# Kernel optimization log

Hardware: AMD Instinct MI355X
Metric: run time of the kernel (lower is better)

## Reference

```python
import jax, jax.numpy as jnp
import numpy as np

EPS = 1e-11

def squash(s, axis=-1):
    sq = jnp.sum(s * s, axis=axis, keepdims=True)
    return (sq / (1.0 + sq)) * s / jnp.sqrt(sq + EPS)

def routing(u_hat, scale, num_iters=3):
    # u_hat: (b, P, J, D); dynamic routing (Sabour et al.), softmax over output capsules J
    b, P, J, D = u_hat.shape
    b_ij = jnp.zeros((b, P, J), u_hat.dtype)
    v = None
    for _ in range(num_iters):
        c = jax.nn.softmax(b_ij, axis=-1)
        s = jnp.einsum('bpj,bpjd->bjd', c, u_hat) / scale
        v = squash(s)
        b_ij = b_ij + jnp.einsum('bpjd,bjd->bpj', u_hat, v)
    return v

def normalize_adj(adj):
    deg = jnp.sum(adj, axis=-1)
    d_inv_sqrt = jnp.where(deg > 0, deg ** -0.5, 0.0)
    return d_inv_sqrt[:, :, None] * adj * d_inv_sqrt[:, None, :]

def setup_inputs():
    key = jax.random.key(0)
    ks = jax.random.split(key, 20)
    b, n = 32, 512
    vocabs = [128, 64, 16]
    emb, C, L = 64, 2, 3
    hidden = emb * C                 # 128
    gcn_in = emb * len(vocabs)       # 192
    att_dim = emb * C * L            # 384
    Jg, Dg = 16, 32                  # num_graph_capsules, graph_embedding_size
    ncls = 6
    recon_hidden = int(gcn_in * 2 / 3)  # 128
    recon_dim = 208
    g = lambda i, *s: jax.random.normal(ks[i], s, jnp.float32) * 0.05
    # sparse symmetric adjacency with self-loops (binary, like real graph data)
    adj = (jax.random.uniform(ks[0], (b, n, n)) < 0.02).astype(jnp.float32)
    adj = jnp.maximum(adj, jnp.swapaxes(adj, 1, 2))
    adj = jnp.maximum(adj, jnp.eye(n, dtype=jnp.float32)[None])
    return {
        'adj': adj,
        'nodes0': jax.random.randint(ks[1], (b, n), 0, vocabs[0]),
        'nodes1': jax.random.randint(ks[2], (b, n), 0, vocabs[1]),
        'nodes2': jax.random.randint(ks[3], (b, n), 0, vocabs[2]),
        'label': jax.random.randint(ks[4], (b,), 0, ncls),
        'reconstructs': jax.random.uniform(ks[5], (b, recon_dim)),
        'emb0': g(6, vocabs[0], emb), 'emb1': g(7, vocabs[1], emb), 'emb2': g(8, vocabs[2], emb),
        'gw0': g(9, gcn_in, hidden), 'gb0': jnp.zeros((hidden,), jnp.float32),
        'gw1': g(10, hidden, hidden), 'gb1': jnp.zeros((hidden,), jnp.float32),
        'gw2': g(11, hidden, hidden), 'gb2': jnp.zeros((hidden,), jnp.float32),
        'aw1': g(12, att_dim, att_dim), 'ab1': jnp.zeros((att_dim,), jnp.float32),
        'aw2': g(13, att_dim, 1), 'ab2': jnp.zeros((1,), jnp.float32),
        'Wg': g(14, C * L, emb, Jg, Dg),
        'Wc': g(15, Jg, Dg, ncls, Dg),
        'rw1': g(16, Dg, recon_hidden), 'rb1': jnp.zeros((recon_hidden,), jnp.float32),
        'rw2': g(17, recon_hidden, recon_dim), 'rb2': jnp.zeros((recon_dim,), jnp.float32),
    }

def reference(adj, nodes0, nodes1, nodes2, label, reconstructs,
              emb0, emb1, emb2, gw0, gb0, gw1, gb1, gw2, gb2,
              aw1, ab1, aw2, ab2, Wg, Wc, rw1, rb1, rw2, rb2):
    b, n, _ = adj.shape
    C = 2
    lambda_val, reg_scale = 0.5, 0.1
    # embeddings (dropout omitted: eval-mode reference)
    feats = jnp.concatenate([emb0[nodes0], emb1[nodes1], emb2[nodes2]], axis=-1)  # (b,n,192)
    masks = jnp.max(adj, axis=-1, keepdims=True)                    # (b,n,1)
    num_nodes = jnp.sum(masks, axis=1, keepdims=True)[..., None]    # (b,1,1,1)
    adj_norm = normalize_adj(adj)
    hid = []
    h = feats
    for W, bb in ((gw0, gb0), (gw1, gb1), (gw2, gb2)):
        h = jnp.tanh(jnp.einsum('bnm,bmd->bnd', adj_norm, h @ W + bb))
        hid.append(h.reshape(b, n, C, -1))
    H = jnp.concatenate(hid, axis=2)                                # (b,n,C*L,emb)
    attn = jnp.tanh(H.reshape(b, n, -1) @ aw1 + ab1) @ aw2 + ab2    # (b,n,1)
    attn = jax.nn.softmax(jnp.where(masks > 0, attn, -jnp.inf), axis=1)[..., None]
    H = H * attn * num_nodes
    # graph capsules: every (node, channel) is an input capsule
    Jg, Dg = Wg.shape[2], Wg.shape[3]
    u_hat = jnp.einsum('bnci,cijd->bncjd', H, Wg).reshape(b, n * Wg.shape[0], Jg, Dg)
    v_g = routing(u_hat, num_nodes.reshape(b, 1, 1))                # (b,Jg,Dg)
    u_hat2 = jnp.einsum('bci,cijd->bcjd', v_g, Wc)
    v_c = routing(u_hat2, 1.0)                                      # (b,ncls,Dg)
    # margin loss
    v_mag = jnp.sqrt(jnp.sum(v_c * v_c, axis=2))
    pred = jnp.argmax(v_mag, axis=1)
    max_l = jnp.maximum(0.9 - v_mag, 0.0) ** 2
    max_r = jnp.maximum(v_mag - 0.1, 0.0) ** 2
    T_c = jax.nn.one_hot(label, v_mag.shape[1], dtype=v_c.dtype)
    L_c = jnp.sum(T_c * max_l + lambda_val * (1.0 - T_c) * max_r, axis=1)
    margin_loss = jnp.mean(L_c)
    # reconstruction loss
    capsule_masked = jnp.sum(v_c * T_c[..., None], axis=1)          # (b,Dg)
    rec = jax.nn.sigmoid(jax.nn.relu(capsule_masked @ rw1 + rb1) @ rw2 + rb2)
    neg_ind = (reconstructs < 1e-05).astype(rec.dtype)
    pos_ind = 1.0 - neg_ind
    rec_val = reconstructs / (jnp.max(reconstructs, axis=1, keepdims=True) + EPS)
    diff = (rec - rec_val) ** 2
    recon_loss = jnp.mean(jnp.max(diff * pos_ind, axis=-1) + jnp.max(diff * neg_ind, axis=-1))
    loss = margin_loss + recon_loss * reg_scale
    return (v_c, loss, margin_loss, recon_loss, pred)
```

## Files before the change

### kernel.cpp

```cpp
#include <hip/hip_runtime.h>
#include <hip/hip_bf16.h>
#include <math.h>

#define NB 32
#define NN 512
#define GIN 192
#define ATT 384
#define EPSF 1e-11f

typedef __attribute__((ext_vector_type(4))) float f32x4;
typedef __attribute__((ext_vector_type(8))) short short8;

__device__ __forceinline__ ushort bfhi(float f) {
    uint u = __float_as_uint(f);
    return (ushort)((u + 0x7FFFu + ((u >> 16) & 1u)) >> 16);
}
__device__ __forceinline__ float bff(ushort h) {
    return __uint_as_float(((uint)h) << 16);
}
__device__ __forceinline__ void bfsplit(float f, ushort& hi, ushort& lo) {
    hi = bfhi(f);
    lo = bfhi(f - bff(hi));
}

__global__ __launch_bounds__(64) void k_prep(const float* __restrict__ adj,
                                             ushort* __restrict__ nbr,
                                             int* __restrict__ deg,
                                             float* __restrict__ dinv,
                                             float* __restrict__ mask) {
    int row = blockIdx.x;
    int t = threadIdx.x;
    const float* a = adj + (size_t)row * NN;
    float4 v0 = ((const float4*)a)[t * 2];
    float4 v1 = ((const float4*)a)[t * 2 + 1];
    float vv[8] = {v0.x, v0.y, v0.z, v0.w, v1.x, v1.y, v1.z, v1.w};
    float s = 0.f, m = 0.f;
    int cnt = 0;
    unsigned long long below = (t == 63) ? 0xFFFFFFFFFFFFFFFFULL >> 1
                                         : ((1ULL << t) - 1ULL);
#pragma unroll
    for (int e = 0; e < 8; e++) {
        float v = vv[e];
        s += v;
        m = fmaxf(m, v);
        bool nz = v != 0.f;
        unsigned long long bm = __ballot(nz);
        int pos = cnt + __popcll(bm & below);
        if (nz && pos < 64) nbr[(size_t)row * 64 + pos] = (ushort)(t * 8 + e);
        cnt += __popcll(bm);
    }
    for (int off = 32; off; off >>= 1) {
        s += __shfl_xor(s, off);
        m = fmaxf(m, __shfl_xor(m, off));
    }
    if (t == 0) {
        deg[row] = cnt < 64 ? cnt : 64;
        dinv[row] = s > 0.f ? 1.0f / sqrtf(s) : 0.f;
        mask[row] = m;
    }
}

__global__ void k_gather(const int* __restrict__ n0, const int* __restrict__ n1,
                         const int* __restrict__ n2, const float* __restrict__ e0,
                         const float* __restrict__ e1, const float* __restrict__ e2,
                         ushort* __restrict__ fh, ushort* __restrict__ fl) {
    int tid = blockIdx.x * 256 + threadIdx.x;
    if (tid >= NB * NN * GIN) return;
    int bn = tid / GIN, f = tid - bn * GIN;
    float v;
    if (f < 64)       v = e0[n0[bn] * 64 + f];
    else if (f < 128) v = e1[n1[bn] * 64 + (f - 64)];
    else              v = e2[n2[bn] * 64 + (f - 128)];
    ushort h, lo;
    bfsplit(v, h, lo);
    fh[tid] = h; fl[tid] = lo;
}

__global__ __launch_bounds__(256) void k_twtall(
    const float* __restrict__ gw0, const float* __restrict__ gw1,
    const float* __restrict__ gw2, const float* __restrict__ aw1,
    ushort* __restrict__ t0h, ushort* __restrict__ t0l,
    ushort* __restrict__ t1h, ushort* __restrict__ t1l,
    ushort* __restrict__ t2h, ushort* __restrict__ t2l,
    ushort* __restrict__ tah, ushort* __restrict__ tal) {
    const float* W; ushort *Th, *Tl; int K, N;
    switch (blockIdx.z) {
        case 0: W = gw0; Th = t0h; Tl = t0l; K = 192; N = 128; break;
        case 1: W = gw1; Th = t1h; Tl = t1l; K = 128; N = 128; break;
        case 2: W = gw2; Th = t2h; Tl = t2l; K = 128; N = 128; break;
        default: W = aw1; Th = tah; Tl = tal; K = 384; N = 384; break;
    }
    int k0 = blockIdx.x * 32, n0 = blockIdx.y * 32;
    if (k0 >= K || n0 >= N) return;
    __shared__ float tile[32][33];
    int t = threadIdx.x, tx = t & 31, ty = t >> 5;
#pragma unroll
    for (int r = 0; r < 4; r++)
        tile[ty + r * 8][tx] = W[(size_t)(k0 + ty + r * 8) * N + n0 + tx];
    __syncthreads();
#pragma unroll
    for (int r = 0; r < 4; r++) {
        int nn = ty + r * 8;
        float v = tile[tx][nn];
        ushort h, lo;
        bfsplit(v, h, lo);
        size_t o = (size_t)(n0 + nn) * K + k0 + tx;
        Th[o] = h; Tl[o] = lo;
    }
}

template <int KK, int EPI>
__global__ __launch_bounds__(256) void k_mfg(
    const ushort* __restrict__ Ah, const ushort* __restrict__ Al, int lda,
    const ushort* __restrict__ Bh, const ushort* __restrict__ Bl,
    const float* __restrict__ bias, const float* __restrict__ dinv,
    float* __restrict__ Of, const float* __restrict__ aw2p) {
    __shared__ ushort Ash[2048], Asl[2048];
    __shared__ ushort Bsh[4096], Bsl[4096];
    __shared__ float ep[(EPI == 0) ? 64 * 128 : 1];
    int t = threadIdx.x;
    int bid = blockIdx.x;
    {
        int q = gridDim.x >> 3;
        bid = (bid & 7) * q + (bid >> 3);
    }
    int m0 = bid * 64;
    int n0 = blockIdx.y * 128;
    int l = t & 63, w = t >> 6, wr = w >> 1, wc = w & 1;
    int rA = t >> 2, kc = t & 3;
    int rB0 = rA, rB1 = rA + 64;
    int lsA  = ((rA >> 4) * 64 + (rA & 15) + kc * 16) * 8;
    int lsB0 = ((rB0 >> 4) * 64 + (rB0 & 15) + kc * 16) * 8;
    int lsB1 = ((rB1 >> 4) * 64 + (rB1 & 15) + kc * 16) * 8;
    f32x4 z = {0.f, 0.f, 0.f, 0.f};
    f32x4 acc[2][4];
#pragma unroll
    for (int i = 0; i < 2; i++)
#pragma unroll
        for (int j = 0; j < 4; j++) acc[i][j] = z;

    short8 pa0, pal0, pb0, pb1, pbl0, pbl1;
    int kof = kc * 8;
    {
        pa0 = *(const short8*)&Ah[(size_t)(m0 + rA) * lda + kof];
        pal0 = *(const short8*)&Al[(size_t)(m0 + rA) * lda + kof];
        pb0 = *(const short8*)&Bh[(size_t)(n0 + rB0) * KK + kof];
        pb1 = *(const short8*)&Bh[(size_t)(n0 + rB1) * KK + kof];
        pbl0 = *(const short8*)&Bl[(size_t)(n0 + rB0) * KK + kof];
        pbl1 = *(const short8*)&Bl[(size_t)(n0 + rB1) * KK + kof];
    }
    for (int k0 = 0; k0 < KK; k0 += 32) {
        *(short8*)&Ash[lsA] = pa0;
        *(short8*)&Asl[lsA] = pal0;
        *(short8*)&Bsh[lsB0] = pb0;
        *(short8*)&Bsh[lsB1] = pb1;
        *(short8*)&Bsl[lsB0] = pbl0;
        *(short8*)&Bsl[lsB1] = pbl1;
        __syncthreads();
        if (k0 + 32 < KK) {
            int kn = k0 + 32 + kof;
            pa0 = *(const short8*)&Ah[(size_t)(m0 + rA) * lda + kn];
            pal0 = *(const short8*)&Al[(size_t)(m0 + rA) * lda + kn];
            pb0 = *(const short8*)&Bh[(size_t)(n0 + rB0) * KK + kn];
            pb1 = *(const short8*)&Bh[(size_t)(n0 + rB1) * KK + kn];
            pbl0 = *(const short8*)&Bl[(size_t)(n0 + rB0) * KK + kn];
            pbl1 = *(const short8*)&Bl[(size_t)(n0 + rB1) * KK + kn];
        }
        short8 ah[2], al[2], bh[4], bl[4];
#pragma unroll
        for (int i = 0; i < 2; i++) {
            ah[i] = *(const short8*)&Ash[((wr * 2 + i) * 64 + l) * 8];
            al[i] = *(const short8*)&Asl[((wr * 2 + i) * 64 + l) * 8];
        }
#pragma unroll
        for (int j = 0; j < 4; j++) {
            bh[j] = *(const short8*)&Bsh[((wc * 4 + j) * 64 + l) * 8];
            bl[j] = *(const short8*)&Bsl[((wc * 4 + j) * 64 + l) * 8];
        }
#pragma unroll
        for (int i = 0; i < 2; i++)
#pragma unroll
            for (int j = 0; j < 4; j++) {
                acc[i][j] = __builtin_amdgcn_mfma_f32_16x16x32_bf16(ah[i], bh[j], acc[i][j], 0, 0, 0);
                acc[i][j] = __builtin_amdgcn_mfma_f32_16x16x32_bf16(ah[i], bl[j], acc[i][j], 0, 0, 0);
                acc[i][j] = __builtin_amdgcn_mfma_f32_16x16x32_bf16(al[i], bh[j], acc[i][j], 0, 0, 0);
            }
        __syncthreads();
    }
    if constexpr (EPI == 3) {
#pragma unroll
        for (int i = 0; i < 2; i++) {
            float rs[4] = {0.f, 0.f, 0.f, 0.f};
#pragma unroll
            for (int j = 0; j < 4; j++) {
                int gc = n0 + (wc * 4 + j) * 16 + (l & 15);
                float bv = bias[gc], wv = aw2p[gc];
#pragma unroll
                for (int r = 0; r < 4; r++)
                    rs[r] += tanhf(acc[i][j][r] + bv) * wv;
            }
#pragma unroll
            for (int r = 0; r < 4; r++) {
                rs[r] += __shfl_xor(rs[r], 1, 16);
                rs[r] += __shfl_xor(rs[r], 2, 16);
                rs[r] += __shfl_xor(rs[r], 4, 16);
                rs[r] += __shfl_xor(rs[r], 8, 16);
            }
            if ((l & 15) == 0) {
                int gr0 = m0 + (wr * 2 + i) * 16 + 4 * (l >> 4);
#pragma unroll
                for (int r = 0; r < 4; r++) atomicAdd(&Of[gr0 + r], rs[r]);
            }
        }
    } else {
#pragma unroll
        for (int i = 0; i < 2; i++)
#pragma unroll
            for (int j = 0; j < 4; j++) {
                int lc = (wc * 4 + j) * 16 + (l & 15);
                int lr0 = (wr * 2 + i) * 16 + 4 * (l >> 4);
                float bv = bias[lc];
#pragma unroll
                for (int r = 0; r < 4; r++)
                    ep[(lr0 + r) * 128 + lc] = (acc[i][j][r] + bv) * dinv[m0 + lr0 + r];
            }
        __syncthreads();
        int row = t >> 2, c0 = (t & 3) * 32;
        size_t ob = (size_t)(m0 + row) * 128 + c0;
#pragma unroll
        for (int k = 0; k < 8; k++)
            ((float4*)&Of[ob])[k] = *(const float4*)&ep[row * 128 + c0 + k * 4];
    }
}

__global__ __launch_bounds__(256) void k_adjsp(const ushort* __restrict__ nbr,
                                               const int* __restrict__ deg,
                                               const float* __restrict__ Y,
                                               const float* __restrict__ dinv,
                                               ushort* __restrict__ Hbh,
                                               ushort* __restrict__ Hbl, int hoff) {
    int bid = blockIdx.x;
    {
        int q = gridDim.x >> 3;
        bid = (bid & 7) * q + (bid >> 3);
    }
    int b = bid >> 5;
    int rg = bid & 31;
    int base = b * NN + rg * 16;
    __shared__ ushort nl[16 * 64];
    __shared__ int dl[16];
    int t = threadIdx.x;
    if (t < 128) *(short8*)&nl[t * 8] = *(const short8*)&nbr[(size_t)base * 64 + t * 8];
    if (t < 16) dl[t] = deg[base + t];
    __syncthreads();
    int row = t >> 4, c0 = (t & 15) * 8;
    const float* yp = Y + (size_t)b * 65536 + c0;
    float acc[8] = {0.f, 0.f, 0.f, 0.f, 0.f, 0.f, 0.f, 0.f};
    int dg = dl[row];
    const ushort* nr = &nl[row * 64];
    for (int q = 0; q < dg; q++) {
        const float4* y = (const float4*)(yp + (int)nr[q] * 128);
        float4 a = y[0], c = y[1];
        acc[0] += a.x; acc[1] += a.y; acc[2] += a.z; acc[3] += a.w;
        acc[4] += c.x; acc[5] += c.y; acc[6] += c.z; acc[7] += c.w;
    }
    float dv = dinv[base + row];
    short8 vh, vl;
#pragma unroll
    for (int c = 0; c < 8; c++) {
        float v = tanhf(acc[c] * dv);
        ushort h, lo;
        bfsplit(v, h, lo);
        vh[c] = (short)h; vl[c] = (short)lo;
    }
    size_t o = (size_t)(base + row) * ATT + hoff + c0;
    *(short8*)&Hbh[o] = vh;
    *(short8*)&Hbl[o] = vl;
}

__global__ __launch_bounds__(512) void k_attnsm(float* __restrict__ logit,
                                                const float* __restrict__ mask,
                                                float* __restrict__ numn) {
    __shared__ float red[8], red2[8], red3[8];
    int b = blockIdx.x, t = threadIdx.x;
    float mk = mask[b * NN + t];
    float x = mk > 0.f ? logit[b * NN + t] : -INFINITY;
    float m = x, nsum = mk;
    for (int off = 32; off; off >>= 1) {
        m = fmaxf(m, __shfl_xor(m, off));
        nsum += __shfl_xor(nsum, off);
    }
    if ((t & 63) == 0) { red[t >> 6] = m; red3[t >> 6] = nsum; }
    __syncthreads();
    float gm = red[0], nn = red3[0];
    for (int i = 1; i < 8; i++) { gm = fmaxf(gm, red[i]); nn += red3[i]; }
    float e = expf(x - gm);
    float s = e;
    for (int off = 32; off; off >>= 1) s += __shfl_xor(s, off);
    if ((t & 63) == 0) red2[t >> 6] = s;
    __syncthreads();
    float gs = 0.f;
    for (int i = 0; i < 8; i++) gs += red2[i];
    logit[b * NN + t] = (e / gs) * nn;
    if (t == 0) numn[b] = nn;
}

__global__ __launch_bounds__(256) void k_Hsum(const ushort* __restrict__ Hh,
                                              const ushort* __restrict__ Hl,
                                              const float* __restrict__ scale,
                                              float* __restrict__ G0) {
    int blk = blockIdx.x;
    int c = blk % 6, b = blk / 6;
    int t = threadIdx.x;
    int i = t & 63, g = t >> 6;
    float s = 0.f;
    for (int n = g * 128; n < g * 128 + 128; n++) {
        size_t o = ((size_t)b * NN + n) * ATT + c * 64 + i;
        s += scale[b * NN + n] * (bff(Hh[o]) + bff(Hl[o]));
    }
    __shared__ float red[256];
    red[t] = s;
    __syncthreads();
    if (t < 128) red[t] += red[t + 128];
    __syncthreads();
    if (t < 64) G0[(size_t)blk * 64 + i] = red[t] + red[t + 64];
}

template <int SRC, bool DOWV>
__global__ __launch_bounds__(256) void k_SVj(const float* __restrict__ gsrc,
                                             const float* __restrict__ Wg,
                                             const float* __restrict__ numn,
                                             float* __restrict__ vg,
                                             float* __restrict__ Wv) {
    int b = blockIdx.x, j = blockIdx.y;
    int t = threadIdx.x;
    __shared__ float Wgl[384 * 33];
    __shared__ float gj[384];
    __shared__ float red[256];
    __shared__ float vvs[32];
    for (int idx = t; idx < 12288; idx += 256) {
        int r = idx >> 5, d = idx & 31;
        Wgl[r * 33 + d] = Wg[(size_t)r * 512 + j * 32 + d];
    }
    for (int r = t; r < 384; r += 256) {
        if constexpr (SRC == 0) {
            gj[r] = gsrc[b * 384 + r] * (1.f / 16.f);
        } else {
            const float* g = gsrc + ((size_t)b * 6 + (r >> 6)) * 4096 + j * 64 + (r & 63);
            gj[r] = g[0] + g[1024] + g[2048] + g[3072];
        }
    }
    __syncthreads();
    int d = t & 31, g8 = t >> 5;
    float pp = 0.f;
#pragma unroll
    for (int k = 0; k < 48; k++) {
        int r = g8 * 48 + k;
        pp += gj[r] * Wgl[r * 33 + d];
    }
    red[t] = pp;
    __syncthreads();
    if (t < 128) red[t] += red[t + 128];
    __syncthreads();
    if (t < 64) red[t] += red[t + 64];
    __syncthreads();
    if (t < 32) {
        float s = (red[t] + red[t + 32]) / numn[b];
        float sq = s * s;
        for (int off = 16; off; off >>= 1) sq += __shfl_xor(sq, off, 32);
        float v = (sq / (1.f + sq)) * s / sqrtf(sq + EPSF);
        vvs[t] = v;
        vg[(size_t)b * 512 + j * 32 + t] = v;
    }
    __syncthreads();
    if constexpr (DOWV) {
        for (int r = t; r < 384; r += 256) {
            float a = 0.f;
#pragma unroll
            for (int d2 = 0; d2 < 32; d2++) a += Wgl[r * 33 + d2] * vvs[d2];
            Wv[(size_t)b * 6144 + (r >> 6) * 1024 + (r & 63) * 16 + j] = a;
        }
    }
}

__global__ __launch_bounds__(256) void k_GsSM(const float* __restrict__ bij,
                                              const ushort* __restrict__ Hh,
                                              const ushort* __restrict__ Hl,
                                              const float* __restrict__ scale,
                                              float* __restrict__ Gs) {
    int blk = blockIdx.x;
    int seg = blk & 3, c = (blk >> 2) % 6, b = blk / 24;
    __shared__ float ct[16 * 16];
    __shared__ float ht[16 * 64];
    int t = threadIdx.x;
    int i = t & 63, j0 = t >> 6;
    float acc[4] = {0.f, 0.f, 0.f, 0.f};
    int n0 = seg * 128;
    for (int nc = 0; nc < 128; nc += 16) {
        {
            int nn = t >> 4;
            float v = bij[(((size_t)b * NN + n0 + nc + nn) * 6 + c) * 16 + (t & 15)];
            float mx = v;
            mx = fmaxf(mx, __shfl_xor(mx, 1, 16));
            mx = fmaxf(mx, __shfl_xor(mx, 2, 16));
            mx = fmaxf(mx, __shfl_xor(mx, 4, 16));
            mx = fmaxf(mx, __shfl_xor(mx, 8, 16));
            float e = expf(v - mx);
            float sm = e;
            sm += __shfl_xor(sm, 1, 16);
            sm += __shfl_xor(sm, 2, 16);
            sm += __shfl_xor(sm, 4, 16);
            sm += __shfl_xor(sm, 8, 16);
            ct[t] = e / sm;
        }
        for (int idx = t; idx < 1024; idx += 256) {
            int nn = idx >> 6, ii = idx & 63;
            int n = n0 + nc + nn;
            size_t o = ((size_t)b * NN + n) * ATT + c * 64 + ii;
            ht[idx] = scale[b * NN + n] * (bff(Hh[o]) + bff(Hl[o]));
        }
        __syncthreads();
        for (int nn = 0; nn < 16; nn++) {
            float hv = ht[nn * 64 + i];
#pragma unroll
            for (int q = 0; q < 4; q++) acc[q] += ct[nn * 16 + j0 * 4 + q] * hv;
        }
        __syncthreads();
    }
#pragma unroll
    for (int q = 0; q < 4; q++) {
        int j = j0 * 4 + q;
        Gs[(((size_t)b * 6 + c) * 4 + seg) * 1024 + j * 64 + i] = acc[q];
    }
}

template <bool ACC>
__global__ __launch_bounds__(256) void k_bup(const ushort* __restrict__ Hh,
                                             const ushort* __restrict__ Hl,
                                             const float* __restrict__ scale,
                                             const float* __restrict__ Wv,
                                             float* __restrict__ bij) {
    int blk = blockIdx.x;
    int b = blk >> 4;
    int n0 = (blk & 15) * 32;
    __shared__ float wl[6144];
    __shared__ float hl[32 * ATT];
    int t = threadIdx.x;
    for (int idx = t; idx < 6144; idx += 256) wl[idx] = Wv[(size_t)b * 6144 + idx];
    for (int idx = t; idx < 32 * ATT; idx += 256) {
        int nn = idx / ATT;
        size_t o = ((size_t)b * NN + n0) * ATT + idx;
        hl[idx] = scale[b * NN + n0 + nn] * (bff(Hh[o]) + bff(Hl[o]));
    }
    __syncthreads();
    for (int idx = t; idx < 3072; idx += 256) {
        int nn = idx / 96, r = idx % 96, c = r >> 4, j = r & 15;
        float a = 0.f;
        const float* h = hl + nn * ATT + c * 64;
        const float* w = wl + c * 1024 + j;
#pragma unroll
        for (int i2 = 0; i2 < 64; i2++) a += h[i2] * w[i2 * 16];
        size_t o = (((size_t)b * NN + n0 + nn) * 6 + c) * 16 + j;
        if constexpr (ACC) bij[o] += a;
        else bij[o] = a;
    }
}

__global__ __launch_bounds__(256) void k_u2(const float* __restrict__ vg,
                                            const float* __restrict__ Wc,
                                            float* __restrict__ u2g) {
    int c = blockIdx.x;
    int t = threadIdx.x;
    __shared__ float Wcl[32 * 192];
    __shared__ float vgl[32 * 32];
    for (int idx = t; idx < 6144; idx += 256)
        Wcl[idx] = Wc[(size_t)c * 6144 + idx];
    for (int idx = t; idx < 1024; idx += 256) {
        int b = idx >> 5, i2 = idx & 31;
        vgl[idx] = vg[(size_t)b * 512 + c * 32 + i2];
    }
    __syncthreads();
    for (int o = t; o < 6144; o += 256) {
        int b = o / 192, jd = o - b * 192;
        float a = 0.f;
#pragma unroll
        for (int i2 = 0; i2 < 32; i2++) a += vgl[b * 32 + i2] * Wcl[i2 * 192 + jd];
        u2g[(size_t)b * 3072 + c * 192 + jd] = a;
    }
}

__global__ __launch_bounds__(256) void k_caps2(
    const float* __restrict__ u2g,
    const int* __restrict__ label, const float* __restrict__ recon_in,
    const float* __restrict__ rw1, const float* __restrict__ rb1,
    const float* __restrict__ rw2, const float* __restrict__ rb2,
    float* __restrict__ out, float* __restrict__ marg, float* __restrict__ reconl) {
    int b = blockIdx.x, t = threadIdx.x;
    __shared__ float u2[3072];
    __shared__ float b2[96], c2b[96];
    __shared__ float vv[192];
    __shared__ float magl[6];
    __shared__ float cm[32];
    __shared__ float hidl[128];
    __shared__ float red[256];
    for (int idx = t; idx < 3072; idx += 256) u2[idx] = u2g[(size_t)b * 3072 + idx];
    if (t < 96) b2[t] = 0.f;
    __syncthreads();
    for (int it = 0; it < 3; it++) {
        if (t < 16) {
            float mx = -INFINITY;
            for (int j = 0; j < 6; j++) mx = fmaxf(mx, b2[t * 6 + j]);
            float e[6], s = 0.f;
            for (int j = 0; j < 6; j++) { e[j] = expf(b2[t * 6 + j] - mx); s += e[j]; }
            for (int j = 0; j < 6; j++) c2b[t * 6 + j] = e[j] / s;
        }
        __syncthreads();
        if (t < 192) {
            int j = t >> 5, d = t & 31;
            float s = 0.f;
            for (int c = 0; c < 16; c++) s += c2b[c * 6 + j] * u2[c * 192 + j * 32 + d];
            float sq = s * s;
            for (int off = 16; off; off >>= 1) sq += __shfl_xor(sq, off, 32);
            vv[t] = (sq / (1.f + sq)) * s / sqrtf(sq + EPSF);
        }
        __syncthreads();
        if (it < 2) {
            if (t < 96) {
                int c = t / 6, j = t - c * 6;
                float a = 0.f;
                for (int d = 0; d < 32; d++) a += u2[c * 192 + j * 32 + d] * vv[j * 32 + d];
                b2[t] += a;
            }
            __syncthreads();
        }
    }
    if (t < 192) out[(size_t)b * 192 + t] = vv[t];
    if (t < 6) {
        float s = 0.f;
        for (int d = 0; d < 32; d++) { float v = vv[t * 32 + d]; s += v * v; }
        magl[t] = sqrtf(s);
    }
    __syncthreads();
    int lab = label[b];
    if (t == 0) {
        float L = 0.f;
        int p = 0;
        float best = magl[0];
        for (int j = 0; j < 6; j++) {
            float mg = magl[j];
            if (mg > best) { best = mg; p = j; }
            float ml = fmaxf(0.9f - mg, 0.f); ml *= ml;
            float mr = fmaxf(mg - 0.1f, 0.f); mr *= mr;
            L += (j == lab) ? ml : 0.5f * mr;
        }
        marg[b] = L;
        out[6147 + b] = (float)p;
    }
    if (t < 32) cm[t] = vv[lab * 32 + t];
    __syncthreads();
    if (t < 128) {
        float a = rb1[t];
        for (int d = 0; d < 32; d++) a += cm[d] * rw1[d * 128 + t];
        hidl[t] = fmaxf(a, 0.f);
    }
    __syncthreads();
    bool act = t < 208;
    float rv = 0.f, rin = 0.f;
    if (act) {
        float a = rb2[t];
        for (int k = 0; k < 128; k++) a += hidl[k] * rw2[k * 208 + t];
        rv = 1.f / (1.f + expf(-a));
        rin = recon_in[(size_t)b * 208 + t];
    }
    red[t] = act ? rin : -INFINITY;
    __syncthreads();
    for (int s2 = 128; s2; s2 >>= 1) {
        if (t < s2) red[t] = fmaxf(red[t], red[t + s2]);
        __syncthreads();
    }
    float rmax = red[0];
    __syncthreads();
    float dpos = 0.f, dneg = 0.f;
    if (act) {
        float rec_val = rin / (rmax + EPSF);
        float d2 = rv - rec_val; d2 *= d2;
        bool neg = rin < 1e-5f;
        dpos = neg ? 0.f : d2;
        dneg = neg ? d2 : 0.f;
    }
    red[t] = dpos;
    __syncthreads();
    for (int s2 = 128; s2; s2 >>= 1) {
        if (t < s2) red[t] = fmaxf(red[t], red[t + s2]);
        __syncthreads();
    }
    float mp = red[0];
    __syncthreads();
    red[t] = dneg;
    __syncthreads();
    for (int s2 = 128; s2; s2 >>= 1) {
        if (t < s2) red[t] = fmaxf(red[t], red[t + s2]);
        __syncthreads();
    }
    if (t == 0) reconl[b] = mp + red[0];
}

__global__ void k_final(const float* __restrict__ marg, const float* __restrict__ reconl,
                        float* __restrict__ out) {
    int t = threadIdx.x;
    float m = (t < 32) ? marg[t] : 0.f;
    float r = (t < 32) ? reconl[t] : 0.f;
    for (int off = 16; off; off >>= 1) { m += __shfl_xor(m, off, 32); r += __shfl_xor(r, off, 32); }
    if (t == 0) {
        m /= 32.f;
        r /= 32.f;
        out[6144] = m + 0.1f * r;
        out[6145] = m;
        out[6146] = r;
    }
}

extern "C" void kernel_launch(void* const* d_in, const int* in_sizes, int n_in,
                              void* d_out, int out_size, void* d_ws, size_t ws_size,
                              hipStream_t stream) {
    const float* adj   = (const float*)d_in[0];
    const int*   n0    = (const int*)d_in[1];
    const int*   n1    = (const int*)d_in[2];
    const int*   n2    = (const int*)d_in[3];
    const int*   label = (const int*)d_in[4];
    const float* recon = (const float*)d_in[5];
    const float* e0    = (const float*)d_in[6];
    const float* e1    = (const float*)d_in[7];
    const float* e2    = (const float*)d_in[8];
    const float* gw0   = (const float*)d_in[9];
    const float* gb0   = (const float*)d_in[10];
    const float* gw1   = (const float*)d_in[11];
    const float* gb1   = (const float*)d_in[12];
    const float* gw2   = (const float*)d_in[13];
    const float* gb2   = (const float*)d_in[14];
    const float* aw1   = (const float*)d_in[15];
    const float* ab1   = (const float*)d_in[16];
    const float* aw2   = (const float*)d_in[17];
    const float* Wg    = (const float*)d_in[19];
    const float* Wc    = (const float*)d_in[20];
    const float* rw1   = (const float*)d_in[21];
    const float* rb1   = (const float*)d_in[22];
    const float* rw2   = (const float*)d_in[23];
    const float* rb2   = (const float*)d_in[24];
    float* out = (float*)d_out;

    char* p = (char*)d_ws;
    auto alloc = [&](size_t bytes) { char* r = p; p += (bytes + 255) & ~(size_t)255; return r; };
    float*  dinv   = (float*)alloc(NB * NN * 4);
    float*  maskp  = (float*)alloc(NB * NN * 4);
    float*  numn   = (float*)alloc(NB * 4);
    float*  logit  = (float*)alloc(NB * NN * 4);
    float*  bij    = (float*)alloc((size_t)NB * NN * 96 * 4);
    float*  Gs     = (float*)alloc((size_t)NB * 24576 * 4);
    float*  G0     = (float*)alloc(NB * 384 * 4);
    float*  vg     = (float*)alloc(NB * 512 * 4);
    float*  Wv     = (float*)alloc(NB * 6144 * 4);
    float*  u2g    = (float*)alloc(NB * 3072 * 4);
    float*  marg   = (float*)alloc(NB * 4);
    float*  recl   = (float*)alloc(NB * 4);
    int*    deg    = (int*)alloc(NB * NN * 4);
    ushort* nbr    = (ushort*)alloc((size_t)NB * NN * 64 * 2);
    ushort* gwt0h  = (ushort*)alloc(128 * 192 * 2);
    ushort* gwt0l  = (ushort*)alloc(128 * 192 * 2);
    ushort* gwt1h  = (ushort*)alloc(128 * 128 * 2);
    ushort* gwt1l  = (ushort*)alloc(128 * 128 * 2);
    ushort* gwt2h  = (ushort*)alloc(128 * 128 * 2);
    ushort* gwt2l  = (ushort*)alloc(128 * 128 * 2);
    ushort* aw1th  = (ushort*)alloc(384 * 384 * 2);
    ushort* aw1tl  = (ushort*)alloc(384 * 384 * 2);
    float*  Ybuf   = (float*)alloc((size_t)NB * NN * 128 * 4);
    ushort* Hbh    = (ushort*)alloc((size_t)NB * NN * ATT * 2);
    ushort* Hbl    = (ushort*)alloc((size_t)NB * NN * ATT * 2);
    ushort* fbh    = (ushort*)alloc((size_t)NB * NN * GIN * 2);
    ushort* fbl    = (ushort*)alloc((size_t)NB * NN * GIN * 2);

    k_prep<<<NB * NN, 64, 0, stream>>>(adj, nbr, deg, dinv, maskp);
    k_gather<<<(NB * NN * GIN + 255) / 256, 256, 0, stream>>>(n0, n1, n2, e0, e1, e2, fbh, fbl);
    k_twtall<<<dim3(12, 12, 4), 256, 0, stream>>>(gw0, gw1, gw2, aw1, gwt0h, gwt0l,
                                                  gwt1h, gwt1l, gwt2h, gwt2l, aw1th, aw1tl);

    k_mfg<192, 0><<<256, 256, 0, stream>>>(fbh, fbl, 192, gwt0h, gwt0l, gb0, dinv, Ybuf, nullptr);
    k_adjsp<<<1024, 256, 0, stream>>>(nbr, deg, Ybuf, dinv, Hbh, Hbl, 0);
    k_mfg<128, 0><<<256, 256, 0, stream>>>(Hbh, Hbl, ATT, gwt1h, gwt1l, gb1, dinv, Ybuf, nullptr);
    k_adjsp<<<1024, 256, 0, stream>>>(nbr, deg, Ybuf, dinv, Hbh, Hbl, 128);
    k_mfg<128, 0><<<256, 256, 0, stream>>>(Hbh + 128, Hbl + 128, ATT, gwt2h, gwt2l, gb2, dinv, Ybuf, nullptr);
    k_adjsp<<<1024, 256, 0, stream>>>(nbr, deg, Ybuf, dinv, Hbh, Hbl, 256);

    hipMemsetAsync(logit, 0, NB * NN * sizeof(float), stream);
    k_mfg<384, 3><<<dim3(256, 3), 256, 0, stream>>>(Hbh, Hbl, ATT, aw1th, aw1tl, ab1, nullptr,
                                                    logit, aw2);
    k_attnsm<<<NB, 512, 0, stream>>>(logit, maskp, numn);

    k_Hsum<<<NB * 6, 256, 0, stream>>>(Hbh, Hbl, logit, G0);
    k_SVj<0, true><<<dim3(NB, 16), 256, 0, stream>>>(G0, Wg, numn, vg, Wv);
    k_bup<false><<<NB * 16, 256, 0, stream>>>(Hbh, Hbl, logit, Wv, bij);
    k_GsSM<<<NB * 24, 256, 0, stream>>>(bij, Hbh, Hbl, logit, Gs);
    k_SVj<1, true><<<dim3(NB, 16), 256, 0, stream>>>(Gs, Wg, numn, vg, Wv);
    k_bup<true><<<NB * 16, 256, 0, stream>>>(Hbh, Hbl, logit, Wv, bij);
    k_GsSM<<<NB * 24, 256, 0, stream>>>(bij, Hbh, Hbl, logit, Gs);
    k_SVj<1, false><<<dim3(NB, 16), 256, 0, stream>>>(Gs, Wg, numn, vg, nullptr);

    k_u2<<<16, 256, 0, stream>>>(vg, Wc, u2g);
    k_caps2<<<NB, 256, 0, stream>>>(u2g, label, recon, rw1, rb1, rw2, rb2, out, marg, recl);
    k_final<<<1, 64, 0, stream>>>(marg, recl, out);
}
```

Baseline: 414.3 us.

## Fuse front-end prep kernels and merge routing tail into one cooperative kernel

```diff
diff --git a/kernel.cpp b/kernel.cpp
--- a/kernel.cpp
+++ b/kernel.cpp
@@ -1,6 +1,9 @@
 #include <hip/hip_runtime.h>
 #include <hip/hip_bf16.h>
+#include <hip/hip_cooperative_groups.h>
 #include <math.h>
+
+namespace cg = cooperative_groups;
 
 #define NB 32
 #define NN 512
@@ -23,89 +26,87 @@
     lo = bfhi(f - bff(hi));
 }
 
-__global__ __launch_bounds__(64) void k_prep(const float* __restrict__ adj,
-                                             ushort* __restrict__ nbr,
-                                             int* __restrict__ deg,
-                                             float* __restrict__ dinv,
-                                             float* __restrict__ mask) {
-    int row = blockIdx.x;
-    int t = threadIdx.x;
-    const float* a = adj + (size_t)row * NN;
-    float4 v0 = ((const float4*)a)[t * 2];
-    float4 v1 = ((const float4*)a)[t * 2 + 1];
-    float vv[8] = {v0.x, v0.y, v0.z, v0.w, v1.x, v1.y, v1.z, v1.w};
-    float s = 0.f, m = 0.f;
-    int cnt = 0;
-    unsigned long long below = (t == 63) ? 0xFFFFFFFFFFFFFFFFULL >> 1
-                                         : ((1ULL << t) - 1ULL);
-#pragma unroll
-    for (int e = 0; e < 8; e++) {
-        float v = vv[e];
-        s += v;
-        m = fmaxf(m, v);
-        bool nz = v != 0.f;
-        unsigned long long bm = __ballot(nz);
-        int pos = cnt + __popcll(bm & below);
-        if (nz && pos < 64) nbr[(size_t)row * 64 + pos] = (ushort)(t * 8 + e);
-        cnt += __popcll(bm);
-    }
-    for (int off = 32; off; off >>= 1) {
-        s += __shfl_xor(s, off);
-        m = fmaxf(m, __shfl_xor(m, off));
-    }
-    if (t == 0) {
-        deg[row] = cnt < 64 ? cnt : 64;
-        dinv[row] = s > 0.f ? 1.0f / sqrtf(s) : 0.f;
-        mask[row] = m;
-    }
-}
-
-__global__ void k_gather(const int* __restrict__ n0, const int* __restrict__ n1,
-                         const int* __restrict__ n2, const float* __restrict__ e0,
-                         const float* __restrict__ e1, const float* __restrict__ e2,
-                         ushort* __restrict__ fh, ushort* __restrict__ fl) {
-    int tid = blockIdx.x * 256 + threadIdx.x;
-    if (tid >= NB * NN * GIN) return;
-    int bn = tid / GIN, f = tid - bn * GIN;
-    float v;
-    if (f < 64)       v = e0[n0[bn] * 64 + f];
-    else if (f < 128) v = e1[n1[bn] * 64 + (f - 64)];
-    else              v = e2[n2[bn] * 64 + (f - 128)];
-    ushort h, lo;
-    bfsplit(v, h, lo);
-    fh[tid] = h; fl[tid] = lo;
-}
-
-__global__ __launch_bounds__(256) void k_twtall(
+__global__ __launch_bounds__(256) void k_front(
+    const float* __restrict__ adj, ushort* __restrict__ nbr, int* __restrict__ deg,
+    float* __restrict__ dinv, float* __restrict__ mask,
+    const int* __restrict__ n0, const int* __restrict__ n1, const int* __restrict__ n2,
+    const float* __restrict__ e0, const float* __restrict__ e1, const float* __restrict__ e2,
+    ushort* __restrict__ fh, ushort* __restrict__ fl,
     const float* __restrict__ gw0, const float* __restrict__ gw1,
     const float* __restrict__ gw2, const float* __restrict__ aw1,
     ushort* __restrict__ t0h, ushort* __restrict__ t0l,
     ushort* __restrict__ t1h, ushort* __restrict__ t1l,
     ushort* __restrict__ t2h, ushort* __restrict__ t2l,
     ushort* __restrict__ tah, ushort* __restrict__ tal) {
-    const float* W; ushort *Th, *Tl; int K, N;
-    switch (blockIdx.z) {
-        case 0: W = gw0; Th = t0h; Tl = t0l; K = 192; N = 128; break;
-        case 1: W = gw1; Th = t1h; Tl = t1l; K = 128; N = 128; break;
-        case 2: W = gw2; Th = t2h; Tl = t2l; K = 128; N = 128; break;
-        default: W = aw1; Th = tah; Tl = tal; K = 384; N = 384; break;
-    }
-    int k0 = blockIdx.x * 32, n0 = blockIdx.y * 32;
-    if (k0 >= K || n0 >= N) return;
     __shared__ float tile[32][33];
-    int t = threadIdx.x, tx = t & 31, ty = t >> 5;
-#pragma unroll
-    for (int r = 0; r < 4; r++)
-        tile[ty + r * 8][tx] = W[(size_t)(k0 + ty + r * 8) * N + n0 + tx];
-    __syncthreads();
-#pragma unroll
-    for (int r = 0; r < 4; r++) {
-        int nn = ty + r * 8;
-        float v = tile[tx][nn];
+    int blk = blockIdx.x, t = threadIdx.x;
+    if (blk < 4096) {
+        int row = blk * 4 + (t >> 6);
+        int lane = t & 63;
+        const float* a = adj + (size_t)row * NN;
+        float4 v0 = ((const float4*)a)[lane * 2];
+        float4 v1 = ((const float4*)a)[lane * 2 + 1];
+        float vv[8] = {v0.x, v0.y, v0.z, v0.w, v1.x, v1.y, v1.z, v1.w};
+        float s = 0.f, m = 0.f;
+        int cnt = 0;
+        unsigned long long below = (lane == 63) ? 0xFFFFFFFFFFFFFFFFULL >> 1
+                                                : ((1ULL << lane) - 1ULL);
+#pragma unroll
+        for (int e = 0; e < 8; e++) {
+            float v = vv[e];
+            s += v;
+            m = fmaxf(m, v);
+            bool nz = v != 0.f;
+            unsigned long long bm = __ballot(nz);
+            int pos = cnt + __popcll(bm & below);
+            if (nz && pos < 64) nbr[(size_t)row * 64 + pos] = (ushort)(lane * 8 + e);
+            cnt += __popcll(bm);
+        }
+        for (int off = 32; off; off >>= 1) {
+            s += __shfl_xor(s, off);
+            m = fmaxf(m, __shfl_xor(m, off));
+        }
+        if (lane == 0) {
+            deg[row] = cnt < 64 ? cnt : 64;
+            dinv[row] = s > 0.f ? 1.0f / sqrtf(s) : 0.f;
+            mask[row] = m;
+        }
+    } else if (blk < 16384) {
+        int tid = (blk - 4096) * 256 + t;
+        int bn = tid / GIN, f = tid - bn * GIN;
+        float v;
+        if (f < 64)       v = e0[n0[bn] * 64 + f];
+        else if (f < 128) v = e1[n1[bn] * 64 + (f - 64)];
+        else              v = e2[n2[bn] * 64 + (f - 128)];
         ushort h, lo;
         bfsplit(v, h, lo);
-        size_t o = (size_t)(n0 + nn) * K + k0 + tx;
-        Th[o] = h; Tl[o] = lo;
+        fh[tid] = h; fl[tid] = lo;
+    } else {
+        int job = blk - 16384;
+        int z = job / 144, rem = job % 144;
+        int k0 = (rem / 12) * 32, nn0 = (rem % 12) * 32;
+        const float* W; ushort *Th, *Tl; int K, N;
+        switch (z) {
+            case 0: W = gw0; Th = t0h; Tl = t0l; K = 192; N = 128; break;
+            case 1: W = gw1; Th = t1h; Tl = t1l; K = 128; N = 128; break;
+            case 2: W = gw2; Th = t2h; Tl = t2l; K = 128; N = 128; break;
+            default: W = aw1; Th = tah; Tl = tal; K = 384; N = 384; break;
+        }
+        if (k0 >= K || nn0 >= N) return;
+        int tx = t & 31, ty = t >> 5;
+#pragma unroll
+        for (int r = 0; r < 4; r++)
+            tile[ty + r * 8][tx] = W[(size_t)(k0 + ty + r * 8) * N + nn0 + tx];
+        __syncthreads();
+#pragma unroll
+        for (int r = 0; r < 4; r++) {
+            int nn = ty + r * 8;
+            float v = tile[tx][nn];
+            ushort h, lo;
+            bfsplit(v, h, lo);
+            size_t o = (size_t)(nn0 + nn) * K + k0 + tx;
+            Th[o] = h; Tl[o] = lo;
+        }
     }
 }
 
@@ -278,76 +279,75 @@
     *(short8*)&Hbl[o] = vl;
 }
 
-__global__ __launch_bounds__(512) void k_attnsm(float* __restrict__ logit,
-                                                const float* __restrict__ mask,
-                                                float* __restrict__ numn) {
-    __shared__ float red[8], red2[8], red3[8];
-    int b = blockIdx.x, t = threadIdx.x;
-    float mk = mask[b * NN + t];
-    float x = mk > 0.f ? logit[b * NN + t] : -INFINITY;
-    float m = x, nsum = mk;
+struct RArgs {
+    float* logit; const float* maskp; float* numn;
+    const ushort* Hbh; const ushort* Hbl;
+    float* G0; const float* Wg; float* vg; float* Wv;
+    float* bij; float* Gs; float* u2g; const float* Wc;
+    const int* label; const float* recon;
+    const float* rw1; const float* rb1; const float* rw2; const float* rb2;
+    float* out; float* marg; float* recl;
+};
+
+__device__ void ph_attnsm(const RArgs& a, int b, int t, float* pool) {
+    float* red = pool; float* red2 = pool + 4; float* red3 = pool + 8;
+    float mk0 = a.maskp[b * NN + t], mk1 = a.maskp[b * NN + 256 + t];
+    float x0 = mk0 > 0.f ? a.logit[b * NN + t] : -INFINITY;
+    float x1 = mk1 > 0.f ? a.logit[b * NN + 256 + t] : -INFINITY;
+    float m = fmaxf(x0, x1), ns = mk0 + mk1;
     for (int off = 32; off; off >>= 1) {
         m = fmaxf(m, __shfl_xor(m, off));
-        nsum += __shfl_xor(nsum, off);
-    }
-    if ((t & 63) == 0) { red[t >> 6] = m; red3[t >> 6] = nsum; }
-    __syncthreads();
-    float gm = red[0], nn = red3[0];
-    for (int i = 1; i < 8; i++) { gm = fmaxf(gm, red[i]); nn += red3[i]; }
-    float e = expf(x - gm);
-    float s = e;
+        ns += __shfl_xor(ns, off);
+    }
+    if ((t & 63) == 0) { red[t >> 6] = m; red3[t >> 6] = ns; }
+    __syncthreads();
+    float gm = fmaxf(fmaxf(red[0], red[1]), fmaxf(red[2], red[3]));
+    float nn = red3[0] + red3[1] + red3[2] + red3[3];
+    float e0 = expf(x0 - gm), e1 = expf(x1 - gm);
+    float s = e0 + e1;
     for (int off = 32; off; off >>= 1) s += __shfl_xor(s, off);
     if ((t & 63) == 0) red2[t >> 6] = s;
     __syncthreads();
-    float gs = 0.f;
-    for (int i = 0; i < 8; i++) gs += red2[i];
-    logit[b * NN + t] = (e / gs) * nn;
-    if (t == 0) numn[b] = nn;
-}
-
-__global__ __launch_bounds__(256) void k_Hsum(const ushort* __restrict__ Hh,
-                                              const ushort* __restrict__ Hl,
-                                              const float* __restrict__ scale,
-                                              float* __restrict__ G0) {
-    int blk = blockIdx.x;
-    int c = blk % 6, b = blk / 6;
-    int t = threadIdx.x;
-    int i = t & 63, g = t >> 6;
+    float gs = red2[0] + red2[1] + red2[2] + red2[3];
+    a.logit[b * NN + t] = (e0 / gs) * nn;
+    a.logit[b * NN + 256 + t] = (e1 / gs) * nn;
+    if (t == 0) a.numn[b] = nn;
+    __syncthreads();
+}
+
+__device__ void ph_Hsum(const RArgs& a, int job, int t, float* pool) {
+    int c = job % 6, b = job / 6;
+    int i = t & 63, gq = t >> 6;
     float s = 0.f;
-    for (int n = g * 128; n < g * 128 + 128; n++) {
+    for (int n = gq * 128; n < gq * 128 + 128; n++) {
         size_t o = ((size_t)b * NN + n) * ATT + c * 64 + i;
-        s += scale[b * NN + n] * (bff(Hh[o]) + bff(Hl[o]));
-    }
-    __shared__ float red[256];
+        s += a.logit[b * NN + n] * (bff(a.Hbh[o]) + bff(a.Hbl[o]));
+    }
+    float* red = pool;
     red[t] = s;
     __syncthreads();
     if (t < 128) red[t] += red[t + 128];
     __syncthreads();
-    if (t < 64) G0[(size_t)blk * 64 + i] = red[t] + red[t + 64];
+    if (t < 64) a.G0[(size_t)job * 64 + i] = red[t] + red[t + 64];
+    __syncthreads();
 }
 
 template <int SRC, bool DOWV>
-__global__ __launch_bounds__(256) void k_SVj(const float* __restrict__ gsrc,
-                                             const float* __restrict__ Wg,
-                                             const float* __restrict__ numn,
-                                             float* __restrict__ vg,
-                                             float* __restrict__ Wv) {
-    int b = blockIdx.x, j = blockIdx.y;
-    int t = threadIdx.x;
-    __shared__ float Wgl[384 * 33];
-    __shared__ float gj[384];
-    __shared__ float red[256];
-    __shared__ float vvs[32];
+__device__ void ph_SVj(const RArgs& a, int b, int j, int t, float* pool) {
+    float* Wgl = pool;
+    float* gj  = pool + 12672;
+    float* red = pool + 13056;
+    float* vvs = pool + 13312;
     for (int idx = t; idx < 12288; idx += 256) {
         int r = idx >> 5, d = idx & 31;
-        Wgl[r * 33 + d] = Wg[(size_t)r * 512 + j * 32 + d];
+        Wgl[r * 33 + d] = a.Wg[(size_t)r * 512 + j * 32 + d];
     }
     for (int r = t; r < 384; r += 256) {
         if constexpr (SRC == 0) {
-            gj[r] = gsrc[b * 384 + r] * (1.f / 16.f);
+            gj[r] = a.G0[b * 384 + r] * (1.f / 16.f);
         } else {
-            const float* g = gsrc + ((size_t)b * 6 + (r >> 6)) * 4096 + j * 64 + (r & 63);
-            gj[r] = g[0] + g[1024] + g[2048] + g[3072];
+            const float* gp = a.Gs + ((size_t)b * 6 + (r >> 6)) * 4096 + j * 64 + (r & 63);
+            gj[r] = gp[0] + gp[1024] + gp[2048] + gp[3072];
         }
     }
     __syncthreads();
@@ -365,41 +365,63 @@
     if (t < 64) red[t] += red[t + 64];
     __syncthreads();
     if (t < 32) {
-        float s = (red[t] + red[t + 32]) / numn[b];
+        float s = (red[t] + red[t + 32]) / a.numn[b];
         float sq = s * s;
         for (int off = 16; off; off >>= 1) sq += __shfl_xor(sq, off, 32);
         float v = (sq / (1.f + sq)) * s / sqrtf(sq + EPSF);
         vvs[t] = v;
-        vg[(size_t)b * 512 + j * 32 + t] = v;
+        a.vg[(size_t)b * 512 + j * 32 + t] = v;
     }
     __syncthreads();
     if constexpr (DOWV) {
         for (int r = t; r < 384; r += 256) {
-            float a = 0.f;
-#pragma unroll
-            for (int d2 = 0; d2 < 32; d2++) a += Wgl[r * 33 + d2] * vvs[d2];
-            Wv[(size_t)b * 6144 + (r >> 6) * 1024 + (r & 63) * 16 + j] = a;
-        }
-    }
-}
-
-__global__ __launch_bounds__(256) void k_GsSM(const float* __restrict__ bij,
-                                              const ushort* __restrict__ Hh,
-                                              const ushort* __restrict__ Hl,
-                                              const float* __restrict__ scale,
-                                              float* __restrict__ Gs) {
-    int blk = blockIdx.x;
-    int seg = blk & 3, c = (blk >> 2) % 6, b = blk / 24;
-    __shared__ float ct[16 * 16];
-    __shared__ float ht[16 * 64];
-    int t = threadIdx.x;
+            float s2 = 0.f;
+#pragma unroll
+            for (int d2 = 0; d2 < 32; d2++) s2 += Wgl[r * 33 + d2] * vvs[d2];
+            a.Wv[(size_t)b * 6144 + (r >> 6) * 1024 + (r & 63) * 16 + j] = s2;
+        }
+    }
+    __syncthreads();
+}
+
+template <bool ACC>
+__device__ void ph_bup16(const RArgs& a, int job, int t, float* pool) {
+    int b = job >> 5;
+    int n0 = (job & 31) * 16;
+    float* wl = pool;
+    float* hl = pool + 6144;
+    for (int idx = t; idx < 6144; idx += 256) wl[idx] = a.Wv[(size_t)b * 6144 + idx];
+    for (int idx = t; idx < 6144; idx += 256) {
+        int nn = idx / ATT;
+        size_t o = ((size_t)b * NN + n0) * ATT + idx;
+        hl[idx] = a.logit[b * NN + n0 + nn] * (bff(a.Hbh[o]) + bff(a.Hbl[o]));
+    }
+    __syncthreads();
+    for (int idx = t; idx < 1536; idx += 256) {
+        int nn = idx / 96, r = idx % 96, c = r >> 4, j = r & 15;
+        float s = 0.f;
+        const float* h = hl + nn * ATT + c * 64;
+        const float* w = wl + c * 1024 + j;
+#pragma unroll
+        for (int i2 = 0; i2 < 64; i2++) s += h[i2] * w[i2 * 16];
+        size_t o = (((size_t)b * NN + n0 + nn) * 6 + c) * 16 + j;
+        if constexpr (ACC) a.bij[o] += s;
+        else a.bij[o] = s;
+    }
+    __syncthreads();
+}
+
+__device__ void ph_GsSM(const RArgs& a, int job, int t, float* pool) {
+    int seg = job & 3, c = (job >> 2) % 6, b = job / 24;
+    float* ct = pool;
+    float* ht = pool + 256;
     int i = t & 63, j0 = t >> 6;
     float acc[4] = {0.f, 0.f, 0.f, 0.f};
     int n0 = seg * 128;
     for (int nc = 0; nc < 128; nc += 16) {
         {
             int nn = t >> 4;
-            float v = bij[(((size_t)b * NN + n0 + nc + nn) * 6 + c) * 16 + (t & 15)];
+            float v = a.bij[(((size_t)b * NN + n0 + nc + nn) * 6 + c) * 16 + (t & 15)];
             float mx = v;
             mx = fmaxf(mx, __shfl_xor(mx, 1, 16));
             mx = fmaxf(mx, __shfl_xor(mx, 2, 16));
@@ -417,7 +439,7 @@
             int nn = idx >> 6, ii = idx & 63;
             int n = n0 + nc + nn;
             size_t o = ((size_t)b * NN + n) * ATT + c * 64 + ii;
-            ht[idx] = scale[b * NN + n] * (bff(Hh[o]) + bff(Hl[o]));
+            ht[idx] = a.logit[b * NN + n] * (bff(a.Hbh[o]) + bff(a.Hbl[o]));
         }
         __syncthreads();
         for (int nn = 0; nn < 16; nn++) {
@@ -430,80 +452,39 @@
 #pragma unroll
     for (int q = 0; q < 4; q++) {
         int j = j0 * 4 + q;
-        Gs[(((size_t)b * 6 + c) * 4 + seg) * 1024 + j * 64 + i] = acc[q];
-    }
-}
-
-template <bool ACC>
-__global__ __launch_bounds__(256) void k_bup(const ushort* __restrict__ Hh,
-                                             const ushort* __restrict__ Hl,
-                                             const float* __restrict__ scale,
-                                             const float* __restrict__ Wv,
-                                             float* __restrict__ bij) {
-    int blk = blockIdx.x;
-    int b = blk >> 4;
-    int n0 = (blk & 15) * 32;
-    __shared__ float wl[6144];
-    __shared__ float hl[32 * ATT];
-    int t = threadIdx.x;
-    for (int idx = t; idx < 6144; idx += 256) wl[idx] = Wv[(size_t)b * 6144 + idx];
-    for (int idx = t; idx < 32 * ATT; idx += 256) {
-        int nn = idx / ATT;
-        size_t o = ((size_t)b * NN + n0) * ATT + idx;
-        hl[idx] = scale[b * NN + n0 + nn] * (bff(Hh[o]) + bff(Hl[o]));
-    }
-    __syncthreads();
-    for (int idx = t; idx < 3072; idx += 256) {
-        int nn = idx / 96, r = idx % 96, c = r >> 4, j = r & 15;
-        float a = 0.f;
-        const float* h = hl + nn * ATT + c * 64;
-        const float* w = wl + c * 1024 + j;
-#pragma unroll
-        for (int i2 = 0; i2 < 64; i2++) a += h[i2] * w[i2 * 16];
-        size_t o = (((size_t)b * NN + n0 + nn) * 6 + c) * 16 + j;
-        if constexpr (ACC) bij[o] += a;
-        else bij[o] = a;
-    }
-}
-
-__global__ __launch_bounds__(256) void k_u2(const float* __restrict__ vg,
-                                            const float* __restrict__ Wc,
-                                            float* __restrict__ u2g) {
-    int c = blockIdx.x;
-    int t = threadIdx.x;
-    __shared__ float Wcl[32 * 192];
-    __shared__ float vgl[32 * 32];
-    for (int idx = t; idx < 6144; idx += 256)
-        Wcl[idx] = Wc[(size_t)c * 6144 + idx];
+        a.Gs[(((size_t)b * 6 + c) * 4 + seg) * 1024 + j * 64 + i] = acc[q];
+    }
+}
+
+__device__ void ph_u2(const RArgs& a, int c, int t, float* pool) {
+    float* Wcl = pool;
+    float* vgl = pool + 6144;
+    for (int idx = t; idx < 6144; idx += 256) Wcl[idx] = a.Wc[(size_t)c * 6144 + idx];
     for (int idx = t; idx < 1024; idx += 256) {
         int b = idx >> 5, i2 = idx & 31;
-        vgl[idx] = vg[(size_t)b * 512 + c * 32 + i2];
+        vgl[idx] = a.vg[(size_t)b * 512 + c * 32 + i2];
     }
     __syncthreads();
     for (int o = t; o < 6144; o += 256) {
         int b = o / 192, jd = o - b * 192;
-        float a = 0.f;
-#pragma unroll
-        for (int i2 = 0; i2 < 32; i2++) a += vgl[b * 32 + i2] * Wcl[i2 * 192 + jd];
-        u2g[(size_t)b * 3072 + c * 192 + jd] = a;
-    }
-}
-
-__global__ __launch_bounds__(256) void k_caps2(
-    const float* __restrict__ u2g,
-    const int* __restrict__ label, const float* __restrict__ recon_in,
-    const float* __restrict__ rw1, const float* __restrict__ rb1,
-    const float* __restrict__ rw2, const float* __restrict__ rb2,
-    float* __restrict__ out, float* __restrict__ marg, float* __restrict__ reconl) {
-    int b = blockIdx.x, t = threadIdx.x;
-    __shared__ float u2[3072];
-    __shared__ float b2[96], c2b[96];
-    __shared__ float vv[192];
-    __shared__ float magl[6];
-    __shared__ float cm[32];
-    __shared__ float hidl[128];
-    __shared__ float red[256];
-    for (int idx = t; idx < 3072; idx += 256) u2[idx] = u2g[(size_t)b * 3072 + idx];
+        float s = 0.f;
+#pragma unroll
+        for (int i2 = 0; i2 < 32; i2++) s += vgl[b * 32 + i2] * Wcl[i2 * 192 + jd];
+        a.u2g[(size_t)b * 3072 + c * 192 + jd] = s;
+    }
+    __syncthreads();
+}
+
+__device__ void ph_caps2(const RArgs& a, int b, int t, float* pool) {
+    float* u2   = pool;
+    float* b2   = pool + 3072;
+    float* c2b  = pool + 3168;
+    float* vv   = pool + 3264;
+    float* magl = pool + 3456;
+    float* cm   = pool + 3462;
+    float* hidl = pool + 3494;
+    float* red  = pool + 3622;
+    for (int idx = t; idx < 3072; idx += 256) u2[idx] = a.u2g[(size_t)b * 3072 + idx];
     if (t < 96) b2[t] = 0.f;
     __syncthreads();
     for (int it = 0; it < 3; it++) {
@@ -527,50 +508,50 @@
         if (it < 2) {
             if (t < 96) {
                 int c = t / 6, j = t - c * 6;
-                float a = 0.f;
-                for (int d = 0; d < 32; d++) a += u2[c * 192 + j * 32 + d] * vv[j * 32 + d];
-                b2[t] += a;
+                float s = 0.f;
+                for (int d = 0; d < 32; d++) s += u2[c * 192 + j * 32 + d] * vv[j * 32 + d];
+                b2[t] += s;
             }
             __syncthreads();
         }
     }
-    if (t < 192) out[(size_t)b * 192 + t] = vv[t];
+    if (t < 192) a.out[(size_t)b * 192 + t] = vv[t];
     if (t < 6) {
         float s = 0.f;
         for (int d = 0; d < 32; d++) { float v = vv[t * 32 + d]; s += v * v; }
         magl[t] = sqrtf(s);
     }
     __syncthreads();
-    int lab = label[b];
+    int lab = a.label[b];
     if (t == 0) {
         float L = 0.f;
-        int p = 0;
+        int pbest = 0;
         float best = magl[0];
         for (int j = 0; j < 6; j++) {
             float mg = magl[j];
-            if (mg > best) { best = mg; p = j; }
+            if (mg > best) { best = mg; pbest = j; }
             float ml = fmaxf(0.9f - mg, 0.f); ml *= ml;
             float mr = fmaxf(mg - 0.1f, 0.f); mr *= mr;
             L += (j == lab) ? ml : 0.5f * mr;
         }
-        marg[b] = L;
-        out[6147 + b] = (float)p;
+        a.marg[b] = L;
+        a.out[6147 + b] = (float)pbest;
     }
     if (t < 32) cm[t] = vv[lab * 32 + t];
     __syncthreads();
     if (t < 128) {
-        float a = rb1[t];
-        for (int d = 0; d < 32; d++) a += cm[d] * rw1[d * 128 + t];
-        hidl[t] = fmaxf(a, 0.f);
+        float s = a.rb1[t];
+        for (int d = 0; d < 32; d++) s += cm[d] * a.rw1[d * 128 + t];
+        hidl[t] = fmaxf(s, 0.f);
     }
     __syncthreads();
     bool act = t < 208;
     float rv = 0.f, rin = 0.f;
     if (act) {
-        float a = rb2[t];
-        for (int k = 0; k < 128; k++) a += hidl[k] * rw2[k * 208 + t];
-        rv = 1.f / (1.f + expf(-a));
-        rin = recon_in[(size_t)b * 208 + t];
+        float s = a.rb2[t];
+        for (int k = 0; k < 128; k++) s += hidl[k] * a.rw2[k * 208 + t];
+        rv = 1.f / (1.f + expf(-s));
+        rin = a.recon[(size_t)b * 208 + t];
     }
     red[t] = act ? rin : -INFINITY;
     __syncthreads();
@@ -602,22 +583,53 @@
         if (t < s2) red[t] = fmaxf(red[t], red[t + s2]);
         __syncthreads();
     }
-    if (t == 0) reconl[b] = mp + red[0];
-}
-
-__global__ void k_final(const float* __restrict__ marg, const float* __restrict__ reconl,
-                        float* __restrict__ out) {
-    int t = threadIdx.x;
-    float m = (t < 32) ? marg[t] : 0.f;
-    float r = (t < 32) ? reconl[t] : 0.f;
-    for (int off = 16; off; off >>= 1) { m += __shfl_xor(m, off, 32); r += __shfl_xor(r, off, 32); }
-    if (t == 0) {
-        m /= 32.f;
-        r /= 32.f;
-        out[6144] = m + 0.1f * r;
-        out[6145] = m;
-        out[6146] = r;
-    }
+    if (t == 0) a.recl[b] = mp + red[0];
+}
+
+__device__ void ph_final(const RArgs& a, int t) {
+    if (t < 32) {
+        float m = a.marg[t], r = a.recl[t];
+        for (int off = 16; off; off >>= 1) {
+            m += __shfl_xor(m, off, 32);
+            r += __shfl_xor(r, off, 32);
+        }
+        if (t == 0) {
+            m /= 32.f;
+            r /= 32.f;
+            a.out[6144] = m + 0.1f * r;
+            a.out[6145] = m;
+            a.out[6146] = r;
+        }
+    }
+}
+
+__global__ __launch_bounds__(256) void k_route(RArgs a) {
+    cg::grid_group grid = cg::this_grid();
+    __shared__ __align__(16) float pool[13344];
+    int blk = blockIdx.x, t = threadIdx.x;
+    if (blk < 32) ph_attnsm(a, blk, t, pool);
+    grid.sync();
+    if (blk < 192) ph_Hsum(a, blk, t, pool);
+    grid.sync();
+    ph_SVj<0, true>(a, blk >> 4, blk & 15, t, pool);
+    grid.sync();
+    for (int job = blk; job < 1024; job += 512) ph_bup16<false>(a, job, t, pool);
+    grid.sync();
+    for (int job = blk; job < 768; job += 512) ph_GsSM(a, job, t, pool);
+    grid.sync();
+    ph_SVj<1, true>(a, blk >> 4, blk & 15, t, pool);
+    grid.sync();
+    for (int job = blk; job < 1024; job += 512) ph_bup16<true>(a, job, t, pool);
+    grid.sync();
+    for (int job = blk; job < 768; job += 512) ph_GsSM(a, job, t, pool);
+    grid.sync();
+    ph_SVj<1, false>(a, blk >> 4, blk & 15, t, pool);
+    grid.sync();
+    if (blk < 16) ph_u2(a, blk, t, pool);
+    grid.sync();
+    if (blk < 32) ph_caps2(a, blk, t, pool);
+    grid.sync();
+    if (blk == 0) ph_final(a, t);
 }
 
 extern "C" void kernel_launch(void* const* d_in, const int* in_sizes, int n_in,
@@ -679,10 +691,11 @@
     ushort* fbh    = (ushort*)alloc((size_t)NB * NN * GIN * 2);
     ushort* fbl    = (ushort*)alloc((size_t)NB * NN * GIN * 2);
 
-    k_prep<<<NB * NN, 64, 0, stream>>>(adj, nbr, deg, dinv, maskp);
-    k_gather<<<(NB * NN * GIN + 255) / 256, 256, 0, stream>>>(n0, n1, n2, e0, e1, e2, fbh, fbl);
-    k_twtall<<<dim3(12, 12, 4), 256, 0, stream>>>(gw0, gw1, gw2, aw1, gwt0h, gwt0l,
-                                                  gwt1h, gwt1l, gwt2h, gwt2l, aw1th, aw1tl);
+    k_front<<<16960, 256, 0, stream>>>(adj, nbr, deg, dinv, maskp,
+                                       n0, n1, n2, e0, e1, e2, fbh, fbl,
+                                       gw0, gw1, gw2, aw1,
+                                       gwt0h, gwt0l, gwt1h, gwt1l,
+                                       gwt2h, gwt2l, aw1th, aw1tl);
 
     k_mfg<192, 0><<<256, 256, 0, stream>>>(fbh, fbl, 192, gwt0h, gwt0l, gb0, dinv, Ybuf, nullptr);
     k_adjsp<<<1024, 256, 0, stream>>>(nbr, deg, Ybuf, dinv, Hbh, Hbl, 0);
@@ -694,18 +707,15 @@
     hipMemsetAsync(logit, 0, NB * NN * sizeof(float), stream);
     k_mfg<384, 3><<<dim3(256, 3), 256, 0, stream>>>(Hbh, Hbl, ATT, aw1th, aw1tl, ab1, nullptr,
                                                     logit, aw2);
-    k_attnsm<<<NB, 512, 0, stream>>>(logit, maskp, numn);
-
-    k_Hsum<<<NB * 6, 256, 0, stream>>>(Hbh, Hbl, logit, G0);
-    k_SVj<0, true><<<dim3(NB, 16), 256, 0, stream>>>(G0, Wg, numn, vg, Wv);
-    k_bup<false><<<NB * 16, 256, 0, stream>>>(Hbh, Hbl, logit, Wv, bij);
-    k_GsSM<<<NB * 24, 256, 0, stream>>>(bij, Hbh, Hbl, logit, Gs);
-    k_SVj<1, true><<<dim3(NB, 16), 256, 0, stream>>>(Gs, Wg, numn, vg, Wv);
-    k_bup<true><<<NB * 16, 256, 0, stream>>>(Hbh, Hbl, logit, Wv, bij);
-    k_GsSM<<<NB * 24, 256, 0, stream>>>(bij, Hbh, Hbl, logit, Gs);
-    k_SVj<1, false><<<dim3(NB, 16), 256, 0, stream>>>(Gs, Wg, numn, vg, nullptr);
-
-    k_u2<<<16, 256, 0, stream>>>(vg, Wc, u2g);
-    k_caps2<<<NB, 256, 0, stream>>>(u2g, label, recon, rw1, rb1, rw2, rb2, out, marg, recl);
-    k_final<<<1, 64, 0, stream>>>(marg, recl, out);
-}
+
+    RArgs ra;
+    ra.logit = logit; ra.maskp = maskp; ra.numn = numn;
+    ra.Hbh = Hbh; ra.Hbl = Hbl;
+    ra.G0 = G0; ra.Wg = Wg; ra.vg = vg; ra.Wv = Wv;
+    ra.bij = bij; ra.Gs = Gs; ra.u2g = u2g; ra.Wc = Wc;
+    ra.label = label; ra.recon = recon;
+    ra.rw1 = rw1; ra.rb1 = rb1; ra.rw2 = rw2; ra.rb2 = rb2;
+    ra.out = out; ra.marg = marg; ra.recl = recl;
+    void* kargs[] = { &ra };
+    hipLaunchCooperativeKernel((void*)k_route, dim3(512), dim3(256), kargs, 0, stream);
+}
```

New measurement: 1.046 ms. +152.6%, slower.
